# Performance work log

Measured on AMD Instinct MI355X. Metric: run time of the kernel, lower is better.

The kernel has to match this reference:

```python
import jax, jax.numpy as jnp
import numpy as np

KS = 3  # kernel_size
N, C_IN, C_OUT, H, W = 8, 64, 128, 256, 256


def _grid_sample_bilinear(img, gx, gy):
    """img [C,H,W]; gx, gy [Ho,Wo] normalized coords; align_corners=False, zero padding."""
    C, H_, W_ = img.shape
    ix = ((gx + 1.0) * W_ - 1.0) / 2.0
    iy = ((gy + 1.0) * H_ - 1.0) / 2.0
    x0 = jnp.floor(ix); y0 = jnp.floor(iy)
    x1 = x0 + 1.0;      y1 = y0 + 1.0
    wx1 = ix - x0; wx0 = 1.0 - wx1
    wy1 = iy - y0; wy0 = 1.0 - wy1

    def gather(yi, xi):
        valid = (xi >= 0) & (xi < W_) & (yi >= 0) & (yi < H_)
        xc = jnp.clip(xi, 0, W_ - 1).astype(jnp.int32)
        yc = jnp.clip(yi, 0, H_ - 1).astype(jnp.int32)
        v = img[:, yc, xc]  # [C,Ho,Wo]
        return v * valid[None].astype(img.dtype)

    out = (gather(y0, x0) * (wy0 * wx0)[None]
         + gather(y0, x1) * (wy0 * wx1)[None]
         + gather(y1, x0) * (wy1 * wx0)[None]
         + gather(y1, x1) * (wy1 * wx1)[None])
    return out


def setup_inputs() -> dict:
    key = jax.random.key(0)
    k1, k2, k3 = jax.random.split(key, 3)
    x = jax.random.normal(k1, (N, C_IN, H, W), dtype=jnp.float32)
    # offset conv: Conv2d(inc, 2*ks, ks, padding=(ks-1)//2, bias=False)
    offset_w = jax.random.normal(k2, (2 * KS, C_IN, KS, KS), dtype=jnp.float32) * 0.05
    # conv_kernel: Conv2d(inc, outc, kernel=(ks,1), stride=(ks,1), bias=False), kaiming fan_out
    fan_out = C_OUT * KS * 1
    conv_w = jax.random.normal(k3, (C_OUT, C_IN, KS, 1), dtype=jnp.float32) * np.sqrt(2.0 / fan_out)
    return {"x": x, "offset_w": offset_w, "conv_w": conv_w}


def reference(x, offset_w, conv_w):
    n, c, h, w = x.shape
    ks = KS
    pad = (ks - 1) // 2
    dn = ('NCHW', 'OIHW', 'NCHW')

    off = jax.lax.conv_general_dilated(x, offset_w, (1, 1), ((pad, pad), (pad, pad)),
                                       dimension_numbers=dn)  # [n,2ks,h,w]
    off = jnp.tanh(off).reshape(n, 2, ks, h, w)
    offset_y = off[:, 0]  # [n,ks,h,w]; x offsets are computed but unused in the original

    yc = (ks - 1) // 2
    # cumulative offsets radiating outward from the center row
    upper = jnp.cumsum(offset_y[:, yc:], axis=1)                       # indices yc..ks-1
    lower = jnp.cumsum(offset_y[:, :yc + 1][:, ::-1], axis=1)[:, ::-1]  # indices 0..yc
    y_new = jnp.concatenate([lower[:, :yc], upper], axis=1)            # [n,ks,h,w]

    # base grid replicates torch's repeat-then-reshape layout exactly:
    # flat pattern [-1,0,1,-1,0,1,...] of length ks*h*w, reshaped to (ks,h,w)
    vals = jnp.arange(-(ks - 1) // 2, (ks - 1) // 2 + 1, dtype=x.dtype)
    base = vals[jnp.arange(ks * h * w) % ks].reshape(ks, h, w)

    grid_y = (base[None] + y_new).reshape(n, ks * h, w)
    gy = grid_y / ((h - 1.0) / 2.0) - 1.0
    gx = jnp.full_like(gy, -1.0)  # grid_x is zeros -> 0/((w-1)/2) - 1 = -1

    sampled = jax.vmap(_grid_sample_bilinear)(x, gx, gy)  # [n,c,ks*h,w]

    out = jax.lax.conv_general_dilated(sampled, conv_w, (ks, 1), ((0, 0), (0, 0)),
                                       dimension_numbers=dn)  # [n,outc,h,w]
    return out
```

## Files before the change

### kernel.cpp

```cpp
#include <hip/hip_runtime.h>
#include <math.h>

#define H 256
#define W 256
#define NB 8
#define CIN 64
#define COUT 128
#define HW (H * W)

typedef float f4v __attribute__((ext_vector_type(4)));

__global__ __launch_bounds__(256) void koffset2(const float* __restrict__ x,
                                                const float* __restrict__ offw,
                                                float* __restrict__ ynew) {
    __shared__ float tile[4][2][10 * 40];
    const int n = blockIdx.z;
    const int i0 = blockIdx.y * 32;
    const int j0 = blockIdx.x * 32;
    const int tid = threadIdx.x;
    const int wv = tid >> 6;
    const int lane = tid & 63;
    const int rloc = lane >> 3;
    const int lj4 = (lane & 7) << 2;
    const int iw0 = i0 + 8 * wv - 1;

    const int a1 = lane / 10, q1 = lane - a1 * 10;
    const int gi1 = iw0 + a1, gj1 = j0 - 4 + 4 * q1;
    const bool v1 = ((unsigned)gi1 < (unsigned)H) && ((unsigned)gj1 < (unsigned)W);
    const size_t off1 = v1 ? ((size_t)gi1 * W + gj1) : 0;

    const int s2 = lane + 64;
    const int a2 = s2 / 10, q2 = s2 - a2 * 10;
    const int gi2 = iw0 + a2, gj2 = j0 - 4 + 4 * q2;
    const bool hv2 = (s2 < 100);
    const bool v2 = hv2 && ((unsigned)gi2 < (unsigned)H) && ((unsigned)gj2 < (unsigned)W);
    const size_t off2 = v2 ? ((size_t)gi2 * W + gj2) : 0;

    const float* xn = x + (size_t)n * CIN * HW;
    const float4 zf4 = make_float4(0.f, 0.f, 0.f, 0.f);

    float4 ra1 = v1 ? *(const float4*)(xn + off1) : zf4;
    float4 ra2 = v2 ? *(const float4*)(xn + off2) : zf4;
    float4 rb1 = v1 ? *(const float4*)(xn + HW + off1) : zf4;
    float4 rb2 = v2 ? *(const float4*)(xn + HW + off2) : zf4;
    const float* p1 = xn + 2 * HW + off1;
    const float* p2 = xn + 2 * HW + off2;

    float acc[3][4];
#pragma unroll
    for (int k = 0; k < 3; ++k)
#pragma unroll
        for (int d = 0; d < 4; ++d) acc[k][d] = 0.f;

    float* buf0 = &tile[wv][0][0];
    float* buf1 = &tile[wv][1][0];

    for (int c = 0; c < CIN; c += 2) {
#pragma unroll
        for (int h = 0; h < 2; ++h) {
            float* buf = h ? buf1 : buf0;
            *(float4*)(buf + 4 * lane) = ra1;
            if (hv2) *(float4*)(buf + 4 * s2) = ra2;
            ra1 = rb1;
            ra2 = rb2;
            if (c + h + 2 < CIN) {
                rb1 = v1 ? *(const float4*)p1 : zf4;
                rb2 = v2 ? *(const float4*)p2 : zf4;
                p1 += HW;
                p2 += HW;
            }
            const float* wp = offw + (size_t)(c + h) * 9;
#pragma unroll
            for (int u = 0; u < 3; ++u) {
                const float* rp = buf + (rloc + u) * 40 + lj4;
                float4 b0 = *(const float4*)(rp);
                float4 b1 = *(const float4*)(rp + 4);
                float4 b2 = *(const float4*)(rp + 8);
                const float r0 = b0.w, r1 = b1.x, r2 = b1.y, r3 = b1.z, r4 = b1.w, r5 = b2.x;
#pragma unroll
                for (int k = 0; k < 3; ++k) {
                    const float w0 = wp[k * 576 + u * 3 + 0];
                    const float w1 = wp[k * 576 + u * 3 + 1];
                    const float w2 = wp[k * 576 + u * 3 + 2];
                    acc[k][0] += r0 * w0 + r1 * w1 + r2 * w2;
                    acc[k][1] += r1 * w0 + r2 * w1 + r3 * w2;
                    acc[k][2] += r2 * w0 + r3 * w1 + r4 * w2;
                    acc[k][3] += r3 * w0 + r4 * w1 + r5 * w2;
                }
            }
        }
    }

    float y[3][4];
#pragma unroll
    for (int d = 0; d < 4; ++d) {
        float t0 = tanhf(acc[0][d]);
        float t1 = tanhf(acc[1][d]);
        float t2 = tanhf(acc[2][d]);
        y[0][d] = t0 + t1;
        y[1][d] = t1;
        y[2][d] = t1 + t2;
    }
    size_t base = (size_t)n * 3 * HW + (size_t)(i0 + 8 * wv + rloc) * W + (j0 + lj4);
#pragma unroll
    for (int k = 0; k < 3; ++k)
        *(float4*)(ynew + base + (size_t)k * HW) =
            make_float4(y[k][0], y[k][1], y[k][2], y[k][3]);
}

__global__ __launch_bounds__(256) void kpmat(const float* __restrict__ x,
                                             const float* __restrict__ convw,
                                             float* __restrict__ P) {
    __shared__ float xl[CIN * 4];
    __shared__ float wl[16 * 192];
    const int n = blockIdx.x >> 3;
    const int co0 = (blockIdx.x & 7) * 16;
    const int tid = threadIdx.x;
    {
        int ci = tid >> 2, y = tid & 3;
        xl[tid] = x[(((size_t)n * CIN + ci) * H + y) * W];
    }
    for (int p = tid; p < 16 * 192; p += 256) wl[p] = convw[co0 * 192 + p];
    __syncthreads();
    if (tid < 192) {
        int co = tid / 12, t = tid - co * 12;
        int r = t >> 2, y = t & 3;
        float s = 0.f;
#pragma unroll
        for (int ci = 0; ci < CIN; ++ci) s += wl[co * 192 + ci * 3 + r] * xl[ci * 4 + y];
        P[((size_t)n * COUT + co0 + co) * 16 + t] = s;
    }
}

__global__ __launch_bounds__(256) void kout(const float* __restrict__ ynew,
                                            const float* __restrict__ P,
                                            float* __restrict__ out) {
    __shared__ float Cs[12 * 256];
    __shared__ float Pl[128 * 16];
    const int n = blockIdx.y;
    const int i = blockIdx.x;
    const int tid = threadIdx.x;

    {
        const f4v* src = (const f4v*)(P + (size_t)n * COUT * 16);
        f4v* dst = (f4v*)Pl;
        dst[tid] = src[tid];
        dst[tid + 256] = src[tid + 256];
    }

    {
        const int j = tid;
        float c[12];
#pragma unroll
        for (int t = 0; t < 12; ++t) c[t] = 0.f;
#pragma unroll
        for (int r = 0; r < 3; ++r) {
            int rowi = 3 * i + r;
            int k = rowi >> 8;
            int i2 = rowi & 255;
            float g = (float)(((k + i2 + j) % 3) - 1) +
                      ynew[((size_t)n * 3 + k) * (H * W) + i2 * W + j];
            float gy = g / 127.5f - 1.0f;
            float iy = ((gy + 1.0f) * 256.0f - 1.0f) * 0.5f;
            float fy = floorf(iy);
            int y0 = (int)fy;
            float w1 = iy - fy;
            if ((unsigned)y0 < 4u) c[r * 4 + y0] += 0.5f * (1.0f - w1);
            int y1 = y0 + 1;
            if ((unsigned)y1 < 4u) c[r * 4 + y1] += 0.5f * w1;
        }
#pragma unroll
        for (int t = 0; t < 12; ++t) Cs[t * 256 + j] = c[t];
    }
    __syncthreads();

    const int jq = (tid & 63) * 4;
    const int cg = tid >> 6;
    float4 cc[12];
#pragma unroll
    for (int t = 0; t < 12; ++t) cc[t] = *(const float4*)&Cs[t * 256 + jq];

    float* op = out + (((size_t)n * COUT) * H + i) * W;
    for (int co = cg * 32; co < cg * 32 + 32; ++co) {
        const float4* pp = (const float4*)&Pl[co * 16];
        float4 P0 = pp[0], P1 = pp[1], P2 = pp[2];
        float pv[12] = {P0.x, P0.y, P0.z, P0.w, P1.x, P1.y, P1.z, P1.w,
                        P2.x, P2.y, P2.z, P2.w};
        f4v a = {0.f, 0.f, 0.f, 0.f};
#pragma unroll
        for (int t = 0; t < 12; ++t) {
            a.x += pv[t] * cc[t].x;
            a.y += pv[t] * cc[t].y;
            a.z += pv[t] * cc[t].z;
            a.w += pv[t] * cc[t].w;
        }
        __builtin_nontemporal_store(a, (f4v*)(op + (size_t)co * (H * W) + jq));
    }
}

extern "C" void kernel_launch(void* const* d_in, const int* in_sizes, int n_in,
                              void* d_out, int out_size, void* d_ws, size_t ws_size,
                              hipStream_t stream) {
    const float* x = (const float*)d_in[0];
    const float* offw = (const float*)d_in[1];
    const float* convw = (const float*)d_in[2];
    float* out = (float*)d_out;

    float* ynew = (float*)d_ws;
    float* P = ynew + (size_t)NB * 3 * HW;

    koffset2<<<dim3(8, 8, NB), 256, 0, stream>>>(x, offw, ynew);
    kpmat<<<dim3(64), 256, 0, stream>>>(x, convw, P);
    kout<<<dim3(H, NB), 256, 0, stream>>>(ynew, P, out);
}
```

Before: 391.2 us.

## Fuse P-matrix kernel into offset conv and replace LDS halo tile with shuffles

Merges the small kpmat kernel into the offset-conv kernel as an extra grid slice (blockIdx.z == NB), which saves one kernel launch. The offset conv no longer stages a 10x40 tile through shared memory. Each lane now loads its three input rows directly as float4 and takes neighbouring columns from adjacent lanes with __shfl, with scalar loads for the edge columns. This removes the LDS writes and reads, but brings redundant global row loads (each row is fetched by three waves' lanes), cross-lane shuffles, and divergent edge handling.

```diff
diff --git a/kernel.cpp b/kernel.cpp
--- a/kernel.cpp
+++ b/kernel.cpp
@@ -10,10 +10,34 @@
 
 typedef float f4v __attribute__((ext_vector_type(4)));
 
-__global__ __launch_bounds__(256) void koffset2(const float* __restrict__ x,
-                                                const float* __restrict__ offw,
-                                                float* __restrict__ ynew) {
-    __shared__ float tile[4][2][10 * 40];
+__global__ __launch_bounds__(256) void kfused(const float* __restrict__ x,
+                                              const float* __restrict__ offw,
+                                              const float* __restrict__ convw,
+                                              float* __restrict__ ynew,
+                                              float* __restrict__ P) {
+    if (blockIdx.z == NB) {
+        __shared__ float xl[CIN * 4];
+        __shared__ float wl[16 * 192];
+        const int n = blockIdx.y;
+        const int co0 = blockIdx.x * 16;
+        const int tid = threadIdx.x;
+        {
+            int ci = tid >> 2, y = tid & 3;
+            xl[tid] = x[(((size_t)n * CIN + ci) * H + y) * W];
+        }
+        for (int p = tid; p < 16 * 192; p += 256) wl[p] = convw[co0 * 192 + p];
+        __syncthreads();
+        if (tid < 192) {
+            int co = tid / 12, t = tid - co * 12;
+            int r = t >> 2, y = t & 3;
+            float s = 0.f;
+#pragma unroll
+            for (int ci = 0; ci < CIN; ++ci) s += wl[co * 192 + ci * 3 + r] * xl[ci * 4 + y];
+            P[((size_t)n * COUT + co0 + co) * 16 + t] = s;
+        }
+        return;
+    }
+
     const int n = blockIdx.z;
     const int i0 = blockIdx.y * 32;
     const int j0 = blockIdx.x * 32;
@@ -21,75 +45,83 @@
     const int wv = tid >> 6;
     const int lane = tid & 63;
     const int rloc = lane >> 3;
-    const int lj4 = (lane & 7) << 2;
-    const int iw0 = i0 + 8 * wv - 1;
-
-    const int a1 = lane / 10, q1 = lane - a1 * 10;
-    const int gi1 = iw0 + a1, gj1 = j0 - 4 + 4 * q1;
-    const bool v1 = ((unsigned)gi1 < (unsigned)H) && ((unsigned)gj1 < (unsigned)W);
-    const size_t off1 = v1 ? ((size_t)gi1 * W + gj1) : 0;
-
-    const int s2 = lane + 64;
-    const int a2 = s2 / 10, q2 = s2 - a2 * 10;
-    const int gi2 = iw0 + a2, gj2 = j0 - 4 + 4 * q2;
-    const bool hv2 = (s2 < 100);
-    const bool v2 = hv2 && ((unsigned)gi2 < (unsigned)H) && ((unsigned)gj2 < (unsigned)W);
-    const size_t off2 = v2 ? ((size_t)gi2 * W + gj2) : 0;
+    const int q = lane & 7;
+    const int orow = i0 + 8 * wv + rloc;
+    const int jq = j0 + q * 4;
+    const int lprev = (lane - 1) & 63;
+    const int lnext = (lane + 1) & 63;
+
+    const bool isq0 = (q == 0), isq7 = (q == 7);
+    const int ecol = isq0 ? (j0 - 1) : (j0 + 32);
+    const bool ecv = (isq0 | isq7) && ((unsigned)ecol < (unsigned)W);
+    const int ecc = ecol < 0 ? 0 : (ecol > W - 1 ? W - 1 : ecol);
+
+    const bool rv0 = (orow >= 1);
+    const bool rv2 = (orow <= H - 2);
+    const size_t ro0 = (size_t)(rv0 ? orow - 1 : 0) * W;
+    const size_t ro1 = (size_t)orow * W;
+    const size_t ro2 = (size_t)(rv2 ? orow + 1 : H - 1) * W;
+    const bool ev0 = rv0 && ecv, ev1 = ecv, ev2 = rv2 && ecv;
 
     const float* xn = x + (size_t)n * CIN * HW;
     const float4 zf4 = make_float4(0.f, 0.f, 0.f, 0.f);
 
-    float4 ra1 = v1 ? *(const float4*)(xn + off1) : zf4;
-    float4 ra2 = v2 ? *(const float4*)(xn + off2) : zf4;
-    float4 rb1 = v1 ? *(const float4*)(xn + HW + off1) : zf4;
-    float4 rb2 = v2 ? *(const float4*)(xn + HW + off2) : zf4;
-    const float* p1 = xn + 2 * HW + off1;
-    const float* p2 = xn + 2 * HW + off2;
-
     float acc[3][4];
 #pragma unroll
     for (int k = 0; k < 3; ++k)
 #pragma unroll
         for (int d = 0; d < 4; ++d) acc[k][d] = 0.f;
 
-    float* buf0 = &tile[wv][0][0];
-    float* buf1 = &tile[wv][1][0];
+#define LOADCH(c, M0, M1, M2, E0, E1, E2)                          \
+    {                                                              \
+        const float* xc = xn + (size_t)(c) * HW;                   \
+        M0 = rv0 ? *(const float4*)(xc + ro0 + jq) : zf4;          \
+        M1 = *(const float4*)(xc + ro1 + jq);                      \
+        M2 = rv2 ? *(const float4*)(xc + ro2 + jq) : zf4;          \
+        E0 = ev0 ? xc[ro0 + ecc] : 0.f;                            \
+        E1 = ev1 ? xc[ro1 + ecc] : 0.f;                            \
+        E2 = ev2 ? xc[ro2 + ecc] : 0.f;                            \
+    }
+
+#define CU(u, M, E)                                                \
+    {                                                              \
+        float lf = __shfl(M.w, lprev);                             \
+        float rt = __shfl(M.x, lnext);                             \
+        if (isq0) lf = E;                                          \
+        if (isq7) rt = E;                                          \
+        const float r0 = lf, r1 = M.x, r2 = M.y, r3 = M.z,         \
+                    r4 = M.w, r5 = rt;                             \
+        _Pragma("unroll") for (int k = 0; k < 3; ++k) {            \
+            const float w0 = wp[k * 576 + (u)*3 + 0];              \
+            const float w1 = wp[k * 576 + (u)*3 + 1];              \
+            const float w2 = wp[k * 576 + (u)*3 + 2];              \
+            acc[k][0] += r0 * w0 + r1 * w1 + r2 * w2;              \
+            acc[k][1] += r1 * w0 + r2 * w1 + r3 * w2;              \
+            acc[k][2] += r2 * w0 + r3 * w1 + r4 * w2;              \
+            acc[k][3] += r3 * w0 + r4 * w1 + r5 * w2;              \
+        }                                                          \
+    }
+
+#define COMPUTE(c, M0, M1, M2, E0, E1, E2)                         \
+    {                                                              \
+        const float* wp = offw + (size_t)(c) * 9;                  \
+        CU(0, M0, E0) CU(1, M1, E1) CU(2, M2, E2)                  \
+    }
+
+    float4 Am0, Am1, Am2, Bm0, Bm1, Bm2;
+    float Ae0, Ae1, Ae2, Be0, Be1, Be2;
+    LOADCH(0, Am0, Am1, Am2, Ae0, Ae1, Ae2);
+    LOADCH(1, Bm0, Bm1, Bm2, Be0, Be1, Be2);
 
     for (int c = 0; c < CIN; c += 2) {
-#pragma unroll
-        for (int h = 0; h < 2; ++h) {
-            float* buf = h ? buf1 : buf0;
-            *(float4*)(buf + 4 * lane) = ra1;
-            if (hv2) *(float4*)(buf + 4 * s2) = ra2;
-            ra1 = rb1;
-            ra2 = rb2;
-            if (c + h + 2 < CIN) {
-                rb1 = v1 ? *(const float4*)p1 : zf4;
-                rb2 = v2 ? *(const float4*)p2 : zf4;
-                p1 += HW;
-                p2 += HW;
-            }
-            const float* wp = offw + (size_t)(c + h) * 9;
-#pragma unroll
-            for (int u = 0; u < 3; ++u) {
-                const float* rp = buf + (rloc + u) * 40 + lj4;
-                float4 b0 = *(const float4*)(rp);
-                float4 b1 = *(const float4*)(rp + 4);
-                float4 b2 = *(const float4*)(rp + 8);
-                const float r0 = b0.w, r1 = b1.x, r2 = b1.y, r3 = b1.z, r4 = b1.w, r5 = b2.x;
-#pragma unroll
-                for (int k = 0; k < 3; ++k) {
-                    const float w0 = wp[k * 576 + u * 3 + 0];
-                    const float w1 = wp[k * 576 + u * 3 + 1];
-                    const float w2 = wp[k * 576 + u * 3 + 2];
-                    acc[k][0] += r0 * w0 + r1 * w1 + r2 * w2;
-                    acc[k][1] += r1 * w0 + r2 * w1 + r3 * w2;
-                    acc[k][2] += r2 * w0 + r3 * w1 + r4 * w2;
-                    acc[k][3] += r3 * w0 + r4 * w1 + r5 * w2;
-                }
-            }
-        }
-    }
+        COMPUTE(c, Am0, Am1, Am2, Ae0, Ae1, Ae2);
+        if (c + 2 < CIN) LOADCH(c + 2, Am0, Am1, Am2, Ae0, Ae1, Ae2);
+        COMPUTE(c + 1, Bm0, Bm1, Bm2, Be0, Be1, Be2);
+        if (c + 3 < CIN) LOADCH(c + 3, Bm0, Bm1, Bm2, Be0, Be1, Be2);
+    }
+#undef LOADCH
+#undef CU
+#undef COMPUTE
 
     float y[3][4];
 #pragma unroll
@@ -101,35 +133,11 @@
         y[1][d] = t1;
         y[2][d] = t1 + t2;
     }
-    size_t base = (size_t)n * 3 * HW + (size_t)(i0 + 8 * wv + rloc) * W + (j0 + lj4);
+    size_t base = (size_t)n * 3 * HW + (size_t)orow * W + jq;
 #pragma unroll
     for (int k = 0; k < 3; ++k)
         *(float4*)(ynew + base + (size_t)k * HW) =
             make_float4(y[k][0], y[k][1], y[k][2], y[k][3]);
-}
-
-__global__ __launch_bounds__(256) void kpmat(const float* __restrict__ x,
-                                             const float* __restrict__ convw,
-                                             float* __restrict__ P) {
-    __shared__ float xl[CIN * 4];
-    __shared__ float wl[16 * 192];
-    const int n = blockIdx.x >> 3;
-    const int co0 = (blockIdx.x & 7) * 16;
-    const int tid = threadIdx.x;
-    {
-        int ci = tid >> 2, y = tid & 3;
-        xl[tid] = x[(((size_t)n * CIN + ci) * H + y) * W];
-    }
-    for (int p = tid; p < 16 * 192; p += 256) wl[p] = convw[co0 * 192 + p];
-    __syncthreads();
-    if (tid < 192) {
-        int co = tid / 12, t = tid - co * 12;
-        int r = t >> 2, y = t & 3;
-        float s = 0.f;
-#pragma unroll
-        for (int ci = 0; ci < CIN; ++ci) s += wl[co * 192 + ci * 3 + r] * xl[ci * 4 + y];
-        P[((size_t)n * COUT + co0 + co) * 16 + t] = s;
-    }
 }
 
 __global__ __launch_bounds__(256) void kout(const float* __restrict__ ynew,
@@ -209,7 +217,6 @@
     float* ynew = (float*)d_ws;
     float* P = ynew + (size_t)NB * 3 * HW;
 
-    koffset2<<<dim3(8, 8, NB), 256, 0, stream>>>(x, offw, ynew);
-    kpmat<<<dim3(64), 256, 0, stream>>>(x, convw, P);
+    kfused<<<dim3(8, 8, NB + 1), 256, 0, stream>>>(x, offw, convw, ynew, P);
     kout<<<dim3(H, NB), 256, 0, stream>>>(ynew, P, out);
 }
```

After: 422.1 us. +7.9%, slower.

## Fuse offset conv and P-matrix kernels with wider block-shared x tiles

Applied to the files above, without the earlier changes.

Merges the offset-conv kernel and the small P-matrix kernel into one launch, using an extra grid z-slice for the P computation. The offset conv now tiles 8x128 output pixels per block, with a block-wide shared tile of 4 channels double-buffered in LDS, instead of per-wave 8x32 tiles of 2 channels. This aims to cut halo over-fetch, amortize register prefetch across more channels, and remove one launch. In exchange it adds a __syncthreads per channel group and uses larger LDS, which may lower occupancy.

```diff
diff --git a/kernel.cpp b/kernel.cpp
--- a/kernel.cpp
+++ b/kernel.cpp
@@ -8,43 +8,84 @@
 #define COUT 128
 #define HW (H * W)
 
+#define TR 8
+#define TC 128
+#define TRH 10
+#define TCS 34
+#define RSTRIDE 140
+#define TILEW (TRH * RSTRIDE)
+#define CPB 4
+#define SLOTS_PER (TRH * TCS)
+#define SLOTS_GRP (CPB * SLOTS_PER)
+
 typedef float f4v __attribute__((ext_vector_type(4)));
 
-__global__ __launch_bounds__(256) void koffset2(const float* __restrict__ x,
-                                                const float* __restrict__ offw,
-                                                float* __restrict__ ynew) {
-    __shared__ float tile[4][2][10 * 40];
+__global__ __launch_bounds__(256) void kfused(const float* __restrict__ x,
+                                              const float* __restrict__ offw,
+                                              const float* __restrict__ convw,
+                                              float* __restrict__ ynew,
+                                              float* __restrict__ P) {
+    __shared__ float smem[2 * CPB * TILEW];
+
+    if (blockIdx.z == NB) {
+        float* xl = smem;
+        float* wl = smem + 256;
+        const int id = blockIdx.y * 2 + blockIdx.x;
+        const int n = id >> 3;
+        const int co0 = (id & 7) * 16;
+        const int tid = threadIdx.x;
+        {
+            int ci = tid >> 2, y = tid & 3;
+            xl[tid] = x[(((size_t)n * CIN + ci) * H + y) * W];
+        }
+        for (int p = tid; p < 16 * 192; p += 256) wl[p] = convw[co0 * 192 + p];
+        __syncthreads();
+        if (tid < 192) {
+            int co = tid / 12, t = tid - co * 12;
+            int r = t >> 2, y = t & 3;
+            float s = 0.f;
+#pragma unroll
+            for (int ci = 0; ci < CIN; ++ci) s += wl[co * 192 + ci * 3 + r] * xl[ci * 4 + y];
+            P[((size_t)n * COUT + co0 + co) * 16 + t] = s;
+        }
+        return;
+    }
+
     const int n = blockIdx.z;
-    const int i0 = blockIdx.y * 32;
-    const int j0 = blockIdx.x * 32;
+    const int i0 = blockIdx.y * TR;
+    const int j0 = blockIdx.x * TC;
     const int tid = threadIdx.x;
-    const int wv = tid >> 6;
-    const int lane = tid & 63;
-    const int rloc = lane >> 3;
-    const int lj4 = (lane & 7) << 2;
-    const int iw0 = i0 + 8 * wv - 1;
-
-    const int a1 = lane / 10, q1 = lane - a1 * 10;
-    const int gi1 = iw0 + a1, gj1 = j0 - 4 + 4 * q1;
-    const bool v1 = ((unsigned)gi1 < (unsigned)H) && ((unsigned)gj1 < (unsigned)W);
-    const size_t off1 = v1 ? ((size_t)gi1 * W + gj1) : 0;
-
-    const int s2 = lane + 64;
-    const int a2 = s2 / 10, q2 = s2 - a2 * 10;
-    const int gi2 = iw0 + a2, gj2 = j0 - 4 + 4 * q2;
-    const bool hv2 = (s2 < 100);
-    const bool v2 = hv2 && ((unsigned)gi2 < (unsigned)H) && ((unsigned)gj2 < (unsigned)W);
-    const size_t off2 = v2 ? ((size_t)gi2 * W + gj2) : 0;
+
+    int pw[6], boff[6];
+    bool val[6], have[6];
+#pragma unroll
+    for (int k = 0; k < 6; ++k) {
+        int s = tid + (k << 8);
+        bool h = s < SLOTS_GRP;
+        have[k] = h;
+        int sc = h ? s : 0;
+        int g = sc / SLOTS_PER;
+        int s3 = sc - g * SLOTS_PER;
+        int a = s3 / TCS;
+        int c4 = s3 - a * TCS;
+        int gi = i0 - 1 + a;
+        int gj = j0 - 4 + (c4 << 2);
+        bool v = h && ((unsigned)gi < (unsigned)H) && ((unsigned)gj <= 252u);
+        val[k] = v;
+        boff[k] = v ? (g * HW + gi * W + gj) : 0;
+        pw[k] = g * TILEW + a * RSTRIDE + (c4 << 2);
+    }
 
     const float* xn = x + (size_t)n * CIN * HW;
     const float4 zf4 = make_float4(0.f, 0.f, 0.f, 0.f);
 
-    float4 ra1 = v1 ? *(const float4*)(xn + off1) : zf4;
-    float4 ra2 = v2 ? *(const float4*)(xn + off2) : zf4;
-    float4 rb1 = v1 ? *(const float4*)(xn + HW + off1) : zf4;
-    float4 rb2 = v2 ? *(const float4*)(xn + HW + off2) : zf4;
-    const float* p1 = xn + 2 * HW + off1;
-    const float* p2 = xn + 2 * HW + off2;
+    float4 RA0, RA1, RA2, RA3, RA4, RA5;
+    RA0 = val[0] ? *(const float4*)(xn + boff[0]) : zf4;
+    RA1 = val[1] ? *(const float4*)(xn + boff[1]) : zf4;
+    RA2 = val[2] ? *(const float4*)(xn + boff[2]) : zf4;
+    RA3 = val[3] ? *(const float4*)(xn + boff[3]) : zf4;
+    RA4 = val[4] ? *(const float4*)(xn + boff[4]) : zf4;
+    RA5 = val[5] ? *(const float4*)(xn + boff[5]) : zf4;
 
     float acc[3][4];
 #pragma unroll
@@ -52,84 +93,69 @@
 #pragma unroll
         for (int d = 0; d < 4; ++d) acc[k][d] = 0.f;
 
-    float* buf0 = &tile[wv][0][0];
-    float* buf1 = &tile[wv][1][0];
-
-    for (int c = 0; c < CIN; c += 2) {
-#pragma unroll
-        for (int h = 0; h < 2; ++h) {
-            float* buf = h ? buf1 : buf0;
-            *(float4*)(buf + 4 * lane) = ra1;
-            if (hv2) *(float4*)(buf + 4 * s2) = ra2;
-            ra1 = rb1;
-            ra2 = rb2;
-            if (c + h + 2 < CIN) {
-                rb1 = v1 ? *(const float4*)p1 : zf4;
-                rb2 = v2 ? *(const float4*)p2 : zf4;
-                p1 += HW;
-                p2 += HW;
-            }
-            const float* wp = offw + (size_t)(c + h) * 9;
+    const int r = tid >> 5;
+    const int qd = tid & 31;
+
+    for (int it = 0; it < 16; ++it) {
+        float* buf = (it & 1) ? (smem + CPB * TILEW) : smem;
+        if (have[0]) *(float4*)(buf + pw[0]) = RA0;
+        if (have[1]) *(float4*)(buf + pw[1]) = RA1;
+        if (have[2]) *(float4*)(buf + pw[2]) = RA2;
+        if (have[3]) *(float4*)(buf + pw[3]) = RA3;
+        if (have[4]) *(float4*)(buf + pw[4]) = RA4;
+        if (have[5]) *(float4*)(buf + pw[5]) = RA5;
+        __syncthreads();
+        __builtin_amdgcn_sched_barrier(0);
+        if (it < 15) {
+            const float* xc = xn + (size_t)((it + 1) * CPB) * HW;
+            RA0 = val[0] ? *(const float4*)(xc + boff[0]) : zf4;
+            RA1 = val[1] ? *(const float4*)(xc + boff[1]) : zf4;
+            RA2 = val[2] ? *(const float4*)(xc + boff[2]) : zf4;
+            RA3 = val[3] ? *(const float4*)(xc + boff[3]) : zf4;
+            RA4 = val[4] ? *(const float4*)(xc + boff[4]) : zf4;
+            RA5 = val[5] ? *(const float4*)(xc + boff[5]) : zf4;
+        }
+        const float* wpc = offw + (size_t)(it * CPB) * 9;
+#pragma unroll
+        for (int cc = 0; cc < CPB; ++cc) {
+            const float* wp = wpc + cc * 9;
+            const float* tb = buf + cc * TILEW + r * RSTRIDE + (qd << 2);
 #pragma unroll
             for (int u = 0; u < 3; ++u) {
-                const float* rp = buf + (rloc + u) * 40 + lj4;
-                float4 b0 = *(const float4*)(rp);
+                const float* rp = tb + u * RSTRIDE;
                 float4 b1 = *(const float4*)(rp + 4);
-                float4 b2 = *(const float4*)(rp + 8);
-                const float r0 = b0.w, r1 = b1.x, r2 = b1.y, r3 = b1.z, r4 = b1.w, r5 = b2.x;
-#pragma unroll
-                for (int k = 0; k < 3; ++k) {
-                    const float w0 = wp[k * 576 + u * 3 + 0];
-                    const float w1 = wp[k * 576 + u * 3 + 1];
-                    const float w2 = wp[k * 576 + u * 3 + 2];
-                    acc[k][0] += r0 * w0 + r1 * w1 + r2 * w2;
-                    acc[k][1] += r1 * w0 + r2 * w1 + r3 * w2;
-                    acc[k][2] += r2 * w0 + r3 * w1 + r4 * w2;
-                    acc[k][3] += r3 * w0 + r4 * w1 + r5 * w2;
+                float e0 = rp[3];
+                float e1 = rp[8];
+                const float r0 = e0, r1 = b1.x, r2 = b1.y, r3 = b1.z,
+                            r4 = b1.w, r5 = e1;
+#pragma unroll
+                for (int kk = 0; kk < 3; ++kk) {
+                    const float w0 = wp[kk * 576 + u * 3 + 0];
+                    const float w1 = wp[kk * 576 + u * 3 + 1];
+                    const float w2 = wp[kk * 576 + u * 3 + 2];
+                    acc[kk][0] += r0 * w0 + r1 * w1 + r2 * w2;
+                    acc[kk][1] += r1 * w0 + r2 * w1 + r3 * w2;
+                    acc[kk][2] += r2 * w0 + r3 * w1 + r4 * w2;
+                    acc[kk][3] += r3 * w0 + r4 * w1 + r5 * w2;
                 }
             }
         }
     }
 
-    float y[3][4];
+    float y0[4], y1[4], y2[4];
 #pragma unroll
     for (int d = 0; d < 4; ++d) {
         float t0 = tanhf(acc[0][d]);
         float t1 = tanhf(acc[1][d]);
         float t2 = tanhf(acc[2][d]);
-        y[0][d] = t0 + t1;
-        y[1][d] = t1;
-        y[2][d] = t1 + t2;
-    }
-    size_t base = (size_t)n * 3 * HW + (size_t)(i0 + 8 * wv + rloc) * W + (j0 + lj4);
-#pragma unroll
-    for (int k = 0; k < 3; ++k)
-        *(float4*)(ynew + base + (size_t)k * HW) =
-            make_float4(y[k][0], y[k][1], y[k][2], y[k][3]);
-}
-
-__global__ __launch_bounds__(256) void kpmat(const float* __restrict__ x,
-                                             const float* __restrict__ convw,
-                                             float* __restrict__ P) {
-    __shared__ float xl[CIN * 4];
-    __shared__ float wl[16 * 192];
-    const int n = blockIdx.x >> 3;
-    const int co0 = (blockIdx.x & 7) * 16;
-    const int tid = threadIdx.x;
-    {
-        int ci = tid >> 2, y = tid & 3;
-        xl[tid] = x[(((size_t)n * CIN + ci) * H + y) * W];
-    }
-    for (int p = tid; p < 16 * 192; p += 256) wl[p] = convw[co0 * 192 + p];
-    __syncthreads();
-    if (tid < 192) {
-        int co = tid / 12, t = tid - co * 12;
-        int r = t >> 2, y = t & 3;
-        float s = 0.f;
-#pragma unroll
-        for (int ci = 0; ci < CIN; ++ci) s += wl[co * 192 + ci * 3 + r] * xl[ci * 4 + y];
-        P[((size_t)n * COUT + co0 + co) * 16 + t] = s;
-    }
+        y0[d] = t0 + t1;
+        y1[d] = t1;
+        y2[d] = t1 + t2;
+    }
+    size_t base = (size_t)n * 3 * HW + (size_t)(i0 + r) * W + (j0 + (qd << 2));
+    *(float4*)(ynew + base) = make_float4(y0[0], y0[1], y0[2], y0[3]);
+    *(float4*)(ynew + base + (size_t)HW) = make_float4(y1[0], y1[1], y1[2], y1[3]);
+    *(float4*)(ynew + base + (size_t)2 * HW) = make_float4(y2[0], y2[1], y2[2], y2[3]);
 }
 
 __global__ __launch_bounds__(256) void kout(const float* __restrict__ ynew,
@@ -154,8 +180,8 @@
 #pragma unroll
         for (int t = 0; t < 12; ++t) c[t] = 0.f;
 #pragma unroll
-        for (int r = 0; r < 3; ++r) {
-            int rowi = 3 * i + r;
+        for (int rr = 0; rr < 3; ++rr) {
+            int rowi = 3 * i + rr;
             int k = rowi >> 8;
             int i2 = rowi & 255;
             float g = (float)(((k + i2 + j) % 3) - 1) +
@@ -165,9 +191,9 @@
             float fy = floorf(iy);
             int y0 = (int)fy;
             float w1 = iy - fy;
-            if ((unsigned)y0 < 4u) c[r * 4 + y0] += 0.5f * (1.0f - w1);
+            if ((unsigned)y0 < 4u) c[rr * 4 + y0] += 0.5f * (1.0f - w1);
             int y1 = y0 + 1;
-            if ((unsigned)y1 < 4u) c[r * 4 + y1] += 0.5f * w1;
+            if ((unsigned)y1 < 4u) c[rr * 4 + y1] += 0.5f * w1;
         }
 #pragma unroll
         for (int t = 0; t < 12; ++t) Cs[t * 256 + j] = c[t];
@@ -209,7 +235,6 @@
     float* ynew = (float*)d_ws;
     float* P = ynew + (size_t)NB * 3 * HW;
 
-    koffset2<<<dim3(8, 8, NB), 256, 0, stream>>>(x, offw, ynew);
-    kpmat<<<dim3(64), 256, 0, stream>>>(x, convw, P);
+    kfused<<<dim3(2, 32, NB + 1), 256, 0, stream>>>(x, offw, convw, ynew, P);
     kout<<<dim3(H, NB), 256, 0, stream>>>(ynew, P, out);
 }
```

New measurement: 402.1 us. 1.03x slower.
